# Optimization experiments

Hardware: AMD Instinct MI355X
Metric: run time of the kernel (lower is better)

The kernel has to match this reference:

```python
import jax, jax.numpy as jnp
import numpy as np

D = 128          # idim == odim
HDIM = 1024
CDIM = 128
N_ITER = HDIM // CDIM   # 8 matching-pursuit iterations
PAD = D - 1
TEMPER = 0.85
ENERGY_TH = 0.01
IGNORE_OUT = 0.0


def pad_for_shift(key):
    # key: (B,T,D) -> (B,T,S,D) windowed shift candidates, S = 2D-1
    key_pad = jnp.pad(key, ((0, 0), (0, 0), (PAD, PAD)))
    win = jnp.arange(2 * D - 1)[:, None] + jnp.arange(D)[None, :]  # (S,D)
    return key_pad[..., win]


def selector(x_aug, y):
    # cosine similarity of each shift candidate against y, argmax over shifts
    num = jnp.einsum('btsd,btd->bts', x_aug, y)
    denom = jnp.linalg.norm(x_aug, axis=-1) * jnp.linalg.norm(y, axis=-1)[..., None]
    sim = jnp.where(denom > 0, num / jnp.maximum(denom, 1e-12), 0.0)
    theta = jnp.argmax(sim, axis=-1)          # (B,T) optimal shift index
    sim_opt = jnp.max(sim, axis=-1)
    y_align = jnp.take_along_axis(x_aug, theta[..., None, None], axis=-2)[..., 0, :]
    return y_align, sim_opt, theta


def attention(x, y):
    return jax.nn.softmax(x * y / TEMPER, axis=-1)


def reverse_pad_for_shift(key, theta):
    # undo the shift selected by theta (data-dependent gather)
    key_pad = jnp.pad(key, ((0, 0), (0, 0), (PAD, PAD)))
    idx = (2 * PAD - theta)[..., None] + jnp.arange(D)  # (B,T,D)
    return jnp.take_along_axis(key_pad, idx, axis=-1)


def disentangle(x, mask_prev, W_enc, W_dec):
    # encode, pick CDIM fresh highest-energy hidden units, decode
    h = jax.nn.relu(x @ W_enc)                      # (B,T,HDIM)
    energy = jnp.mean(h * h, axis=(0, 1))           # (HDIM,)
    avail = jnp.where(mask_prev > 0, -jnp.inf, energy)
    _, idx = jax.lax.top_k(avail, CDIM)
    mask_cur = jnp.zeros((HDIM,), h.dtype).at[idx].set(1.0)
    h_sel = h * mask_cur
    out = h_sel @ W_dec
    loss_h = jnp.mean((h - h_sel) ** 2)
    return out, mask_prev + mask_cur, loss_h


def seq_energy_loss(pred, target, seq_mask, th):
    energy = jnp.mean(target * target, axis=-1)     # (B,T)
    valid = (~seq_mask) & (energy > th)[..., None]
    diff = (pred - target) ** 2 * valid
    return jnp.sum(diff) / jnp.maximum(jnp.sum(valid), 1)


def setup_inputs() -> dict:
    key = jax.random.key(0)
    k1, k2, k3, k4 = jax.random.split(key, 4)
    B, T = 8, 512
    return {
        'x': jax.random.normal(k1, (B, T, D), jnp.float32),
        'y': jax.random.normal(k2, (B, T, D), jnp.float32),
        'W_enc': jax.random.normal(k3, (D, HDIM), jnp.float32) / np.sqrt(D),
        'W_dec': jax.random.normal(k4, (HDIM, D), jnp.float32) / np.sqrt(HDIM),
    }


def reference(x, y, W_enc, W_dec):
    seq_mask = (y == IGNORE_OUT)
    y_res, x_res = y, x
    mask_prev = jnp.zeros((HDIM,), x.dtype)
    losses = []
    for _ in range(N_ITER):
        x_aug = pad_for_shift(x_res)                        # (B,T,2D-1,D)
        y_align_opt, sim_opt, theta = selector(x_aug, y_res)
        attn = attention(y_align_opt, y_res)
        y_align_opt_attn = y_align_opt * attn
        x_ele = reverse_pad_for_shift(y_align_opt_attn, theta)
        y_ele, mask_prev, loss_h = disentangle(y_align_opt_attn, mask_prev, W_enc, W_dec)
        loss_local = seq_energy_loss(y_ele, y_res, seq_mask, ENERGY_TH)
        losses.append(loss_local + loss_h)
        # .detach() in original -> stop_gradient on residuals
        y_res = jax.lax.stop_gradient(y_res - y_ele)
        x_res = jax.lax.stop_gradient(x_res - x_ele)
    return jnp.mean(jnp.stack(losses))
```

## Files before the change

kernel.cpp:

```cpp
#include <hip/hip_runtime.h>
#include <math.h>

#define DD 128
#define SS 255
#define HDIM 1024
#define CDIM 128
#define NPOS 4096
#define TEMPER 0.85f
#define ENERGY_TH 0.01f

__global__ __launch_bounds__(256) void k_init(const float* __restrict__ x, const float* __restrict__ y,
                                              float* __restrict__ xr, float* __restrict__ yr,
                                              float* __restrict__ energy, float* __restrict__ maskp,
                                              float* __restrict__ scal) {
    int gid = blockIdx.x * 256 + threadIdx.x;
    for (int i = gid; i < NPOS * DD; i += gridDim.x * 256) { xr[i] = x[i]; yr[i] = y[i]; }
    if (gid < HDIM) { energy[gid] = 0.f; maskp[gid] = 0.f; }
    if (gid < 8)    { scal[gid] = 0.f; }
}

__global__ __launch_bounds__(256) void k_align(float* __restrict__ xr_g, const float* __restrict__ yr_g,
                                               float* __restrict__ V_g) {
    __shared__ __align__(16) float xsp[4][384];
    __shared__ __align__(16) float vpad[4][384];
    __shared__ __align__(16) float ysl[4][128];
    __shared__ float Pfl[4][128];

    const int t = threadIdx.x;
    const int w = t >> 6;
    const int l = t & 63;
    const int pos = blockIdx.x * 4 + w;

    float* xs = xsp[w];
    float* vp = vpad[w];
    float* yw = ysl[w];
    float* pf = Pfl[w];

    for (int i = l; i < 127; i += 64) { xs[i] = 0.f; vp[i] = 0.f; }
    for (int i = 255 + l; i < 384; i += 64) { xs[i] = 0.f; vp[i] = 0.f; }

    const float2 x2 = *(const float2*)(xr_g + pos * DD + 2 * l);
    const float2 y2 = *(const float2*)(yr_g + pos * DD + 2 * l);
    xs[127 + 2 * l] = x2.x; xs[128 + 2 * l] = x2.y;
    yw[2 * l] = y2.x; yw[2 * l + 1] = y2.y;

    float a = x2.x * x2.x, b = x2.y * x2.y;
    float c = a + b;
    #pragma unroll
    for (int off = 1; off < 64; off <<= 1) {
        float n = __shfl_up(c, off);
        if (l >= off) c += n;
    }
    float excl = c - (a + b);
    pf[2 * l]     = excl + a;
    pf[2 * l + 1] = c;

    float yn = y2.x * y2.x + y2.y * y2.y;
    #pragma unroll
    for (int off = 32; off > 0; off >>= 1) yn += __shfl_xor(yn, off);

    __syncthreads();

    float acc0 = 0.f, acc1 = 0.f, acc2 = 0.f, acc3 = 0.f;
    const float4* xs4 = (const float4*)(xs + 4 * l);
    const float4* yw4 = (const float4*)yw;
    float4 xa = xs4[0];
    #pragma unroll 4
    for (int j = 0; j < 32; ++j) {
        float4 xb = xs4[j + 1];
        float4 yv = yw4[j];
        acc0 = fmaf(xa.x, yv.x, fmaf(xa.y, yv.y, fmaf(xa.z, yv.z, fmaf(xa.w, yv.w, acc0))));
        acc1 = fmaf(xa.y, yv.x, fmaf(xa.z, yv.y, fmaf(xa.w, yv.z, fmaf(xb.x, yv.w, acc1))));
        acc2 = fmaf(xa.z, yv.x, fmaf(xa.w, yv.y, fmaf(xb.x, yv.z, fmaf(xb.y, yv.w, acc2))));
        acc3 = fmaf(xa.w, yv.x, fmaf(xb.x, yv.y, fmaf(xb.y, yv.z, fmaf(xb.z, yv.w, acc3))));
        xa = xb;
    }

    float best = -INFINITY; int bidx = 0;
    float accs[4] = {acc0, acc1, acc2, acc3};
    #pragma unroll
    for (int k = 0; k < 4; ++k) {
        int s = 4 * l + k;
        float nrm2 = pf[s < DD ? s : DD - 1] - ((s >= DD) ? pf[s - DD] : 0.f);
        nrm2 = fmaxf(nrm2, 0.f);
        float denom = sqrtf(nrm2) * sqrtf(yn);
        float sim = (denom > 0.f) ? accs[k] / fmaxf(denom, 1e-12f) : 0.f;
        if (s == SS) sim = -INFINITY;
        if (sim > best) { best = sim; bidx = s; }
    }
    #pragma unroll
    for (int off = 32; off > 0; off >>= 1) {
        float ov = __shfl_xor(best, off);
        int   oi = __shfl_xor(bidx, off);
        if (ov > best || (ov == best && oi < bidx)) { best = ov; bidx = oi; }
    }
    const int theta = bidx;

    const int d0 = l, d1 = l + 64;
    float ya0 = xs[theta + d0], ya1 = xs[theta + d1];
    float z0 = ya0 * yw[d0] / TEMPER;
    float z1 = ya1 * yw[d1] / TEMPER;
    float zm = fmaxf(z0, z1);
    #pragma unroll
    for (int off = 32; off > 0; off >>= 1) zm = fmaxf(zm, __shfl_xor(zm, off));
    float e0 = expf(z0 - zm), e1 = expf(z1 - zm);
    float es = e0 + e1;
    #pragma unroll
    for (int off = 32; off > 0; off >>= 1) es += __shfl_xor(es, off);
    float v0 = ya0 * (e0 / es);
    float v1 = ya1 * (e1 / es);
    vp[127 + d0] = v0;
    vp[127 + d1] = v1;
    V_g[pos * DD + d0] = v0;
    V_g[pos * DD + d1] = v1;

    __syncthreads();

    float xe0 = vp[d0 + 2 * (DD - 1) - theta];
    float xe1 = vp[d1 + 2 * (DD - 1) - theta];
    xr_g[pos * DD + d0] = xs[127 + d0] - xe0;
    xr_g[pos * DD + d1] = xs[127 + d1] - xe1;
}

#define MT 64
__global__ __launch_bounds__(256) void k_energy(const float* __restrict__ V_g, const float* __restrict__ We,
                                                float* __restrict__ energy) {
    __shared__ __align__(16) float Vl[MT][DD];
    const int t  = threadIdx.x;
    const int tx = t & 63;
    const int ty = t >> 6;
    const int m0 = blockIdx.x * MT;
    const int n0 = blockIdx.y * 256;
    const int j  = n0 + tx * 4;
    const int r0 = ty * 16;

    const float4* v4 = (const float4*)(V_g + m0 * DD);
    float4* vl4 = (float4*)(&Vl[0][0]);
    #pragma unroll
    for (int i = 0; i < 8; ++i) vl4[t + 256 * i] = v4[t + 256 * i];
    __syncthreads();

    float acc[16][4];
    #pragma unroll
    for (int r = 0; r < 16; ++r)
        #pragma unroll
        for (int cc = 0; cc < 4; ++cc) acc[r][cc] = 0.f;

    for (int d0 = 0; d0 < DD; d0 += 4) {
        float wreg[4][4];
        #pragma unroll
        for (int dd = 0; dd < 4; ++dd) {
            float4 wa = *(const float4*)(We + (d0 + dd) * HDIM + j);
            wreg[dd][0] = wa.x; wreg[dd][1] = wa.y; wreg[dd][2] = wa.z; wreg[dd][3] = wa.w;
        }
        #pragma unroll
        for (int r = 0; r < 16; ++r) {
            float4 v = *(const float4*)(&Vl[r0 + r][d0]);
            float vv[4] = {v.x, v.y, v.z, v.w};
            #pragma unroll
            for (int dd = 0; dd < 4; ++dd)
                #pragma unroll
                for (int cc = 0; cc < 4; ++cc)
                    acc[r][cc] = fmaf(vv[dd], wreg[dd][cc], acc[r][cc]);
        }
    }

    __syncthreads();
    float* Ps = &Vl[0][0];
    #pragma unroll
    for (int cc = 0; cc < 4; ++cc) {
        float e = 0.f;
        #pragma unroll
        for (int r = 0; r < 16; ++r) { float h = fmaxf(acc[r][cc], 0.f); e = fmaf(h, h, e); }
        Ps[ty * 256 + tx * 4 + cc] = e;
    }
    __syncthreads();
    float esum = 0.f;
    #pragma unroll
    for (int q = 0; q < 4; ++q) esum += Ps[q * 256 + t];
    atomicAdd(&energy[n0 + t], esum);
}

__global__ __launch_bounds__(1024) void k_select(float* __restrict__ energy, float* __restrict__ maskp,
                                                 float* __restrict__ scal,
                                                 const float* __restrict__ We, const float* __restrict__ Wd,
                                                 float* __restrict__ Wes, float* __restrict__ Wds, int iter) {
    __shared__ float sv[HDIM];
    __shared__ int   si[HDIM];
    __shared__ int   mk[HDIM];
    __shared__ float red[HDIM];
    __shared__ int   sel_l[CDIM];

    const int t = threadIdx.x;
    if (t == 0) {
        if (iter > 0) scal[3] += scal[0] / fmaxf(scal[1], 1.f) + scal[2];
        scal[0] = 0.f; scal[1] = 0.f;
    }
    float e = energy[t] * (1.0f / (float)NPOS);
    sv[t] = (maskp[t] > 0.f) ? -INFINITY : e;
    si[t] = t;
    __syncthreads();

    for (int k = 2; k <= HDIM; k <<= 1) {
        for (int j = k >> 1; j > 0; j >>= 1) {
            int ixj = t ^ j;
            if (ixj > t) {
                bool up = ((t & k) == 0);
                float va = sv[t], vb = sv[ixj];
                int ia = si[t], ib = si[ixj];
                bool inorder = (va > vb) || (va == vb && ia < ib);
                if (up != inorder) { sv[t] = vb; si[t] = ib; sv[ixj] = va; si[ixj] = ia; }
            }
            __syncthreads();
        }
    }

    mk[t] = 0;
    __syncthreads();
    if (t < CDIM) { mk[si[t]] = 1; sel_l[t] = si[t]; }
    __syncthreads();
    const int mym = mk[t];

    red[t] = e;
    __syncthreads();
    for (int off = 512; off > 0; off >>= 1) { if (t < off) red[t] += red[t + off]; __syncthreads(); }
    const float sum_all = red[0];
    __syncthreads();
    red[t] = mym ? e : 0.f;
    __syncthreads();
    for (int off = 512; off > 0; off >>= 1) { if (t < off) red[t] += red[t + off]; __syncthreads(); }
    const float sum_sel = red[0];
    if (t == 0) scal[2] = (sum_all - sum_sel) / (float)HDIM;

    maskp[t] = maskp[t] + (float)mym;
    energy[t] = 0.f;
    __syncthreads();

    for (int i = t; i < DD * CDIM; i += HDIM) {
        int d = i >> 7, kk = i & 127;
        Wes[i] = We[d * HDIM + sel_l[kk]];
    }
    for (int i = t; i < CDIM * DD; i += HDIM) {
        int kk = i >> 7, d = i & 127;
        Wds[i] = Wd[sel_l[kk] * DD + d];
    }
}

#define RT 32
__global__ __launch_bounds__(256) void k_decode(const float* __restrict__ V_g, const float* __restrict__ Wes,
                                                const float* __restrict__ Wds, float* __restrict__ yr_g,
                                                const float* __restrict__ y_orig, float* __restrict__ scal) {
    __shared__ __align__(16) float Vl[RT][DD];
    __shared__ __align__(16) float Hs[RT][CDIM];
    __shared__ float ren[RT];
    __shared__ float redf[256];

    const int t = threadIdx.x;
    const int r0 = blockIdx.x * RT;

    const float4* v4 = (const float4*)(V_g + r0 * DD);
    float4* vl4 = (float4*)(&Vl[0][0]);
    #pragma unroll
    for (int i = 0; i < 4; ++i) vl4[t + 256 * i] = v4[t + 256 * i];

    {
        int r = t >> 3, lane8 = t & 7;
        float s = 0.f;
        const float* yp = yr_g + (r0 + r) * DD + lane8 * 16;
        #pragma unroll
        for (int c = 0; c < 16; ++c) { float v = yp[c]; s = fmaf(v, v, s); }
        s += __shfl_xor(s, 1); s += __shfl_xor(s, 2); s += __shfl_xor(s, 4);
        if (lane8 == 0) ren[r] = s * (1.f / (float)DD);
    }
    __syncthreads();

    const int half = t >> 7;
    const int k = t & 127;

    {
        float acc[16];
        #pragma unroll
        for (int r = 0; r < 16; ++r) acc[r] = 0.f;
        for (int d0 = 0; d0 < DD; d0 += 4) {
            float w0 = Wes[(d0 + 0) * CDIM + k];
            float w1 = Wes[(d0 + 1) * CDIM + k];
            float w2 = Wes[(d0 + 2) * CDIM + k];
            float w3 = Wes[(d0 + 3) * CDIM + k];
            #pragma unroll
            for (int r = 0; r < 16; ++r) {
                float4 v = *(const float4*)(&Vl[half * 16 + r][d0]);
                acc[r] = fmaf(v.x, w0, fmaf(v.y, w1, fmaf(v.z, w2, fmaf(v.w, w3, acc[r]))));
            }
        }
        #pragma unroll
        for (int r = 0; r < 16; ++r) Hs[half * 16 + r][k] = fmaxf(acc[r], 0.f);
    }
    __syncthreads();

    {
        float acc[16];
        #pragma unroll
        for (int r = 0; r < 16; ++r) acc[r] = 0.f;
        for (int k0 = 0; k0 < CDIM; k0 += 4) {
            float w0 = Wds[(k0 + 0) * DD + k];
            float w1 = Wds[(k0 + 1) * DD + k];
            float w2 = Wds[(k0 + 2) * DD + k];
            float w3 = Wds[(k0 + 3) * DD + k];
            #pragma unroll
            for (int r = 0; r < 16; ++r) {
                float4 h = *(const float4*)(&Hs[half * 16 + r][k0]);
                acc[r] = fmaf(h.x, w0, fmaf(h.y, w1, fmaf(h.z, w2, fmaf(h.w, w3, acc[r]))));
            }
        }
        float sd = 0.f, svld = 0.f;
        #pragma unroll
        for (int r = 0; r < 16; ++r) {
            int row = r0 + half * 16 + r;
            float tgt = yr_g[row * DD + k];
            float yo  = y_orig[row * DD + k];
            bool valid = (yo != 0.f) && (ren[half * 16 + r] > ENERGY_TH);
            float diff = acc[r] - tgt;
            if (valid) { sd = fmaf(diff, diff, sd); svld += 1.f; }
            yr_g[row * DD + k] = tgt - acc[r];
        }
        redf[t] = sd;
        __syncthreads();
        for (int off = 128; off > 0; off >>= 1) { if (t < off) redf[t] += redf[t + off]; __syncthreads(); }
        if (t == 0) atomicAdd(&scal[0], redf[0]);
        __syncthreads();
        redf[t] = svld;
        __syncthreads();
        for (int off = 128; off > 0; off >>= 1) { if (t < off) redf[t] += redf[t + off]; __syncthreads(); }
        if (t == 0) atomicAdd(&scal[1], redf[0]);
    }
}

__global__ void k_final(const float* __restrict__ scal, float* __restrict__ out) {
    float total = scal[3] + scal[0] / fmaxf(scal[1], 1.f) + scal[2];
    out[0] = total * (1.f / 8.f);
}

extern "C" void kernel_launch(void* const* d_in, const int* in_sizes, int n_in,
                              void* d_out, int out_size, void* d_ws, size_t ws_size,
                              hipStream_t stream) {
    const float* x  = (const float*)d_in[0];
    const float* y  = (const float*)d_in[1];
    const float* We = (const float*)d_in[2];
    const float* Wd = (const float*)d_in[3];

    float* ws     = (float*)d_ws;
    float* xr     = ws;
    float* yr     = ws + 524288;
    float* V      = ws + 1048576;
    float* Wes    = ws + 1572864;
    float* Wds    = ws + 1589248;
    float* energy = ws + 1605632;
    float* maskp  = ws + 1606656;
    float* scal   = ws + 1607808;
    float* out    = (float*)d_out;

    k_init<<<2048, 256, 0, stream>>>(x, y, xr, yr, energy, maskp, scal);
    for (int it = 0; it < 8; ++it) {
        k_align<<<NPOS / 4, 256, 0, stream>>>(xr, yr, V);
        k_energy<<<dim3(NPOS / MT, HDIM / 256), 256, 0, stream>>>(V, We, energy);
        k_select<<<1, 1024, 0, stream>>>(energy, maskp, scal, We, Wd, Wes, Wds, it);
        k_decode<<<NPOS / RT, 256, 0, stream>>>(V, Wes, Wds, yr, y, scal);
    }
    k_final<<<1, 1, 0, stream>>>(scal, out);
}
```

Baseline: 728.5 us.

## Fuse all matching-pursuit iterations into one cooperative persistent kernel

Replaces the per-iteration launches of align, energy, select and decode with a single cooperative kernel of 256 blocks that uses grid.sync between phases. Each block owns 16 rows, so V stays in shared memory instead of round-tripping through global memory. Top-k is done in parallel by rank counting across blocks, and energy, mask and loss buffers are double-buffered by iteration parity. This removes around 33 kernel launches and the single-block select bottleneck. In exchange it adds grid-wide barriers and gives the energy GEMM only 256 blocks, each with large per-thread register accumulators. A fallback path keeps the old multi-kernel sequence if the cooperative launch fails.

Result: slower. 1.141 ms (+56.6%).

```diff
diff --git a/kernel.cpp b/kernel.cpp
--- a/kernel.cpp
+++ b/kernel.cpp
@@ -1,5 +1,8 @@
 #include <hip/hip_runtime.h>
+#include <hip/hip_cooperative_groups.h>
 #include <math.h>
+
+namespace cg = cooperative_groups;
 
 #define DD 128
 #define SS 255
@@ -8,6 +11,312 @@
 #define NPOS 4096
 #define TEMPER 0.85f
 #define ENERGY_TH 0.01f
+#define NBLK 256
+#define RPB 16
+
+__global__ __launch_bounds__(256)
+void k_mega(const float* __restrict__ x, const float* __restrict__ y,
+            const float* __restrict__ We, const float* __restrict__ Wd,
+            float* __restrict__ xr, float* __restrict__ yr,
+            float* __restrict__ Wes, float* __restrict__ Wds,
+            float* __restrict__ energy,
+            float* __restrict__ maskp,
+            float* __restrict__ scal,
+            unsigned int* __restrict__ selcnt,
+            float* __restrict__ out)
+{
+    cg::grid_group grid = cg::this_grid();
+    const int b = blockIdx.x;
+    const int t = threadIdx.x;
+    const int w = t >> 6, l = t & 63;
+
+    __shared__ __align__(16) float Vl[RPB][DD];
+    __shared__ __align__(16) float xsp[4][384];
+    __shared__ __align__(16) float vpad[4][384];
+    __shared__ __align__(16) float ysl[4][128];
+    __shared__ float Pfl[4][128];
+    __shared__ __align__(16) float Hs[RPB][CDIM];
+    __shared__ float ren[RPB];
+    __shared__ float redl[8];
+    __shared__ float avL[HDIM];
+    __shared__ unsigned int rkL[4];
+    __shared__ int selSlot[4];
+    __shared__ int selFlag[4];
+
+    {
+        const int r0 = b * RPB;
+        const float4* xs4g = (const float4*)(x + (size_t)r0 * DD);
+        const float4* ys4g = (const float4*)(y + (size_t)r0 * DD);
+        float4* xr4 = (float4*)(xr + (size_t)r0 * DD);
+        float4* yr4 = (float4*)(yr + (size_t)r0 * DD);
+        xr4[t] = xs4g[t]; xr4[t + 256] = xs4g[t + 256];
+        yr4[t] = ys4g[t]; yr4[t + 256] = ys4g[t + 256];
+        if (t < 4) {
+            energy[0 * HDIM + 4 * b + t] = 0.f;
+            energy[1 * HDIM + 4 * b + t] = 0.f;
+            maskp[1 * HDIM + 4 * b + t] = 0.f;
+        }
+        if (b == 0) {
+            if (t < 8) scal[t] = 0.f;
+            if (t < 2) selcnt[t] = 0u;
+        }
+    }
+    grid.sync();
+
+    for (int it = 0; it < 8; ++it) {
+        const int p = it & 1, pp = p ^ 1;
+
+        float* xs = xsp[w]; float* vp = vpad[w]; float* yw = ysl[w]; float* pf = Pfl[w];
+        for (int i = l; i < 127; i += 64)        { xs[i] = 0.f; vp[i] = 0.f; }
+        for (int i = 255 + l; i < 384; i += 64)  { xs[i] = 0.f; vp[i] = 0.f; }
+
+        for (int pq = 0; pq < 4; ++pq) {
+            const int r = 4 * w + pq;
+            const int pos = b * RPB + r;
+            const float2 x2 = *(const float2*)(xr + (size_t)pos * DD + 2 * l);
+            const float2 y2 = *(const float2*)(yr + (size_t)pos * DD + 2 * l);
+            xs[127 + 2 * l] = x2.x; xs[128 + 2 * l] = x2.y;
+            yw[2 * l] = y2.x; yw[2 * l + 1] = y2.y;
+
+            float a = x2.x * x2.x, bb = x2.y * x2.y;
+            float c = a + bb;
+            #pragma unroll
+            for (int off = 1; off < 64; off <<= 1) {
+                float n = __shfl_up(c, off);
+                if (l >= off) c += n;
+            }
+            float excl = c - (a + bb);
+            pf[2 * l] = excl + a;
+            pf[2 * l + 1] = c;
+            float ynv = y2.x * y2.x + y2.y * y2.y;
+            #pragma unroll
+            for (int off = 32; off > 0; off >>= 1) ynv += __shfl_xor(ynv, off);
+            __syncthreads();
+
+            float acc0 = 0.f, acc1 = 0.f, acc2 = 0.f, acc3 = 0.f;
+            const float4* xs4 = (const float4*)(xs + 4 * l);
+            const float4* yw4 = (const float4*)yw;
+            float4 xa = xs4[0];
+            #pragma unroll 4
+            for (int j = 0; j < 32; ++j) {
+                float4 xb = xs4[j + 1];
+                float4 yv = yw4[j];
+                acc0 = fmaf(xa.x, yv.x, fmaf(xa.y, yv.y, fmaf(xa.z, yv.z, fmaf(xa.w, yv.w, acc0))));
+                acc1 = fmaf(xa.y, yv.x, fmaf(xa.z, yv.y, fmaf(xa.w, yv.z, fmaf(xb.x, yv.w, acc1))));
+                acc2 = fmaf(xa.z, yv.x, fmaf(xa.w, yv.y, fmaf(xb.x, yv.z, fmaf(xb.y, yv.w, acc2))));
+                acc3 = fmaf(xa.w, yv.x, fmaf(xb.x, yv.y, fmaf(xb.y, yv.z, fmaf(xb.z, yv.w, acc3))));
+                xa = xb;
+            }
+            float best = -INFINITY; int bidx = 0;
+            float accs[4] = {acc0, acc1, acc2, acc3};
+            #pragma unroll
+            for (int q = 0; q < 4; ++q) {
+                int s = 4 * l + q;
+                float nrm2 = pf[s < DD ? s : DD - 1] - ((s >= DD) ? pf[s - DD] : 0.f);
+                nrm2 = fmaxf(nrm2, 0.f);
+                float denom = sqrtf(nrm2) * sqrtf(ynv);
+                float sim = (denom > 0.f) ? accs[q] / fmaxf(denom, 1e-12f) : 0.f;
+                if (s == SS) sim = -INFINITY;
+                if (sim > best) { best = sim; bidx = s; }
+            }
+            #pragma unroll
+            for (int off = 32; off > 0; off >>= 1) {
+                float ov = __shfl_xor(best, off);
+                int   oi = __shfl_xor(bidx, off);
+                if (ov > best || (ov == best && oi < bidx)) { best = ov; bidx = oi; }
+            }
+            const int theta = bidx;
+
+            float ya0 = xs[theta + l], ya1 = xs[theta + l + 64];
+            float z0 = ya0 * yw[l] / TEMPER;
+            float z1 = ya1 * yw[l + 64] / TEMPER;
+            float zm = fmaxf(z0, z1);
+            #pragma unroll
+            for (int off = 32; off > 0; off >>= 1) zm = fmaxf(zm, __shfl_xor(zm, off));
+            float e0 = expf(z0 - zm), e1 = expf(z1 - zm);
+            float es = e0 + e1;
+            #pragma unroll
+            for (int off = 32; off > 0; off >>= 1) es += __shfl_xor(es, off);
+            float v0 = ya0 * (e0 / es);
+            float v1 = ya1 * (e1 / es);
+            vp[127 + l] = v0; vp[127 + l + 64] = v1;
+            Vl[r][l] = v0;    Vl[r][l + 64] = v1;
+            __syncthreads();
+
+            float xe0 = vp[l + 2 * (DD - 1) - theta];
+            float xe1 = vp[l + 64 + 2 * (DD - 1) - theta];
+            xr[(size_t)pos * DD + l]      = xs[127 + l] - xe0;
+            xr[(size_t)pos * DD + l + 64] = xs[127 + l + 64] - xe1;
+        }
+        __syncthreads();
+
+        {
+            float acc[RPB][4];
+            #pragma unroll
+            for (int r = 0; r < RPB; ++r)
+                #pragma unroll
+                for (int cc = 0; cc < 4; ++cc) acc[r][cc] = 0.f;
+
+            for (int d0 = 0; d0 < DD; d0 += 4) {
+                float4 wr[4];
+                #pragma unroll
+                for (int dd = 0; dd < 4; ++dd)
+                    wr[dd] = *(const float4*)(We + (size_t)(d0 + dd) * HDIM + 4 * t);
+                #pragma unroll
+                for (int r = 0; r < RPB; ++r) {
+                    float4 v = *(const float4*)(&Vl[r][d0]);
+                    const float vv[4] = {v.x, v.y, v.z, v.w};
+                    #pragma unroll
+                    for (int dd = 0; dd < 4; ++dd) {
+                        const float* wp = (const float*)&wr[dd];
+                        #pragma unroll
+                        for (int cc = 0; cc < 4; ++cc)
+                            acc[r][cc] = fmaf(vv[dd], wp[cc], acc[r][cc]);
+                    }
+                }
+            }
+            #pragma unroll
+            for (int cc = 0; cc < 4; ++cc) {
+                float e = 0.f;
+                #pragma unroll
+                for (int r = 0; r < RPB; ++r) { float h = fmaxf(acc[r][cc], 0.f); e = fmaf(h, h, e); }
+                atomicAdd(&energy[p * HDIM + 4 * t + cc], e);
+            }
+        }
+        grid.sync();
+
+        {
+            for (int i = t; i < HDIM; i += 256) {
+                float e = energy[p * HDIM + i];
+                float m = maskp[pp * HDIM + i];
+                avL[i] = (m > 0.f) ? -INFINITY : e;
+            }
+            if (t < 4) rkL[t] = 0u;
+            __syncthreads();
+
+            const int i0 = 4 * b;
+            unsigned int cnt[4] = {0u, 0u, 0u, 0u};
+            const float av0 = avL[i0], av1 = avL[i0 + 1], av2 = avL[i0 + 2], av3 = avL[i0 + 3];
+            #pragma unroll
+            for (int jj = 0; jj < 4; ++jj) {
+                int j = t + 256 * jj;
+                float aj = avL[j];
+                cnt[0] += (aj > av0) || (aj == av0 && j < i0);
+                cnt[1] += (aj > av1) || (aj == av1 && j < i0 + 1);
+                cnt[2] += (aj > av2) || (aj == av2 && j < i0 + 2);
+                cnt[3] += (aj > av3) || (aj == av3 && j < i0 + 3);
+            }
+            #pragma unroll
+            for (int q = 0; q < 4; ++q) if (cnt[q]) atomicAdd(&rkL[q], cnt[q]);
+            __syncthreads();
+
+            if (t < 4) {
+                const int i = i0 + t;
+                const bool masked = (avL[i] == -INFINITY);
+                const bool sel = (rkL[t] < 128u) && !masked;
+                maskp[p * HDIM + i] = (masked || sel) ? 1.f : 0.f;
+                energy[pp * HDIM + i] = 0.f;
+                int slot = -1;
+                if (sel) slot = (int)atomicAdd(&selcnt[p], 1u);
+                selFlag[t] = sel ? 1 : 0;
+                selSlot[t] = slot;
+                if (!sel) atomicAdd(&scal[4 + p], energy[p * HDIM + i]);
+            }
+            if (b == 0 && t == 0) {
+                scal[6] += scal[0 + pp] / fmaxf(scal[2 + pp], 1.f)
+                         + scal[4 + pp] * (1.f / (4096.f * 1024.f));
+                scal[0 + pp] = 0.f; scal[2 + pp] = 0.f; scal[4 + pp] = 0.f;
+                selcnt[pp] = 0u;
+            }
+            __syncthreads();
+
+            #pragma unroll
+            for (int q = 0; q < 4; ++q) {
+                if (selFlag[q]) {
+                    const int i = i0 + q, slot = selSlot[q];
+                    if (t < 128) Wes[(size_t)t * CDIM + slot] = We[(size_t)t * HDIM + i];
+                    else { int d = t - 128; Wds[(size_t)slot * DD + d] = Wd[(size_t)i * DD + d]; }
+                }
+            }
+        }
+        grid.sync();
+
+        {
+            const int r0g = b * RPB;
+            {
+                int r = t >> 4, ln = t & 15;
+                float s = 0.f;
+                const float* yp = yr + (size_t)(r0g + r) * DD + ln * 8;
+                #pragma unroll
+                for (int cci = 0; cci < 8; ++cci) { float v = yp[cci]; s = fmaf(v, v, s); }
+                s += __shfl_xor(s, 1); s += __shfl_xor(s, 2);
+                s += __shfl_xor(s, 4); s += __shfl_xor(s, 8);
+                if (ln == 0) ren[r] = s * (1.f / (float)DD);
+            }
+            const int k = t & 127, rg = t >> 7;
+
+            float acc1[8];
+            #pragma unroll
+            for (int r = 0; r < 8; ++r) acc1[r] = 0.f;
+            for (int d0 = 0; d0 < DD; d0 += 4) {
+                float w0 = Wes[(size_t)(d0 + 0) * CDIM + k];
+                float w1 = Wes[(size_t)(d0 + 1) * CDIM + k];
+                float w2 = Wes[(size_t)(d0 + 2) * CDIM + k];
+                float w3 = Wes[(size_t)(d0 + 3) * CDIM + k];
+                #pragma unroll
+                for (int r = 0; r < 8; ++r) {
+                    float4 v = *(const float4*)(&Vl[rg * 8 + r][d0]);
+                    acc1[r] = fmaf(v.x, w0, fmaf(v.y, w1, fmaf(v.z, w2, fmaf(v.w, w3, acc1[r]))));
+                }
+            }
+            #pragma unroll
+            for (int r = 0; r < 8; ++r) Hs[rg * 8 + r][k] = fmaxf(acc1[r], 0.f);
+            __syncthreads();
+
+            float acc2[8];
+            #pragma unroll
+            for (int r = 0; r < 8; ++r) acc2[r] = 0.f;
+            for (int k0 = 0; k0 < CDIM; k0 += 4) {
+                float w0 = Wds[(size_t)(k0 + 0) * DD + k];
+                float w1 = Wds[(size_t)(k0 + 1) * DD + k];
+                float w2 = Wds[(size_t)(k0 + 2) * DD + k];
+                float w3 = Wds[(size_t)(k0 + 3) * DD + k];
+                #pragma unroll
+                for (int r = 0; r < 8; ++r) {
+                    float4 h = *(const float4*)(&Hs[rg * 8 + r][k0]);
+                    acc2[r] = fmaf(h.x, w0, fmaf(h.y, w1, fmaf(h.z, w2, fmaf(h.w, w3, acc2[r]))));
+                }
+            }
+            float sd = 0.f, sv = 0.f;
+            #pragma unroll
+            for (int r = 0; r < 8; ++r) {
+                const int row = r0g + rg * 8 + r;
+                float tgt = yr[(size_t)row * DD + k];
+                float yo  = y [(size_t)row * DD + k];
+                bool valid = (yo != 0.f) && (ren[rg * 8 + r] > ENERGY_TH);
+                float diff = acc2[r] - tgt;
+                if (valid) { sd = fmaf(diff, diff, sd); sv += 1.f; }
+                yr[(size_t)row * DD + k] = tgt - acc2[r];
+            }
+            #pragma unroll
+            for (int off = 32; off > 0; off >>= 1) { sd += __shfl_xor(sd, off); sv += __shfl_xor(sv, off); }
+            if (l == 0) { redl[w] = sd; redl[4 + w] = sv; }
+            __syncthreads();
+            if (t == 0) {
+                atomicAdd(&scal[0 + p], redl[0] + redl[1] + redl[2] + redl[3]);
+                atomicAdd(&scal[2 + p], redl[4] + redl[5] + redl[6] + redl[7]);
+            }
+            __threadfence_block();
+            __syncthreads();
+        }
+    }
+    grid.sync();
+    if (b == 0 && t == 0) {
+        float total = scal[6] + scal[1] / fmaxf(scal[3], 1.f)
+                    + scal[5] * (1.f / (4096.f * 1024.f));
+        out[0] = total * 0.125f;
+    }
+}
 
 __global__ __launch_bounds__(256) void k_init(const float* __restrict__ x, const float* __restrict__ y,
                                               float* __restrict__ xr, float* __restrict__ yr,
@@ -27,14 +336,10 @@
     __shared__ float Pfl[4][128];
 
     const int t = threadIdx.x;
-    const int w = t >> 6;
-    const int l = t & 63;
+    const int w = t >> 6, l = t & 63;
     const int pos = blockIdx.x * 4 + w;
 
-    float* xs = xsp[w];
-    float* vp = vpad[w];
-    float* yw = ysl[w];
-    float* pf = Pfl[w];
+    float* xs = xsp[w]; float* vp = vpad[w]; float* yw = ysl[w]; float* pf = Pfl[w];
 
     for (int i = l; i < 127; i += 64) { xs[i] = 0.f; vp[i] = 0.f; }
     for (int i = 255 + l; i < 384; i += 64) { xs[i] = 0.f; vp[i] = 0.f; }
@@ -52,13 +357,12 @@
         if (l >= off) c += n;
     }
     float excl = c - (a + b);
-    pf[2 * l]     = excl + a;
+    pf[2 * l] = excl + a;
     pf[2 * l + 1] = c;
 
     float yn = y2.x * y2.x + y2.y * y2.y;
     #pragma unroll
     for (int off = 32; off > 0; off >>= 1) yn += __shfl_xor(yn, off);
-
     __syncthreads();
 
     float acc0 = 0.f, acc1 = 0.f, acc2 = 0.f, acc3 = 0.f;
@@ -79,12 +383,12 @@
     float best = -INFINITY; int bidx = 0;
     float accs[4] = {acc0, acc1, acc2, acc3};
     #pragma unroll
-    for (int k = 0; k < 4; ++k) {
-        int s = 4 * l + k;
+    for (int q = 0; q < 4; ++q) {
+        int s = 4 * l + q;
         float nrm2 = pf[s < DD ? s : DD - 1] - ((s >= DD) ? pf[s - DD] : 0.f);
         nrm2 = fmaxf(nrm2, 0.f);
         float denom = sqrtf(nrm2) * sqrtf(yn);
-        float sim = (denom > 0.f) ? accs[k] / fmaxf(denom, 1e-12f) : 0.f;
+        float sim = (denom > 0.f) ? accs[q] / fmaxf(denom, 1e-12f) : 0.f;
         if (s == SS) sim = -INFINITY;
         if (sim > best) { best = sim; bidx = s; }
     }
@@ -109,11 +413,8 @@
     for (int off = 32; off > 0; off >>= 1) es += __shfl_xor(es, off);
     float v0 = ya0 * (e0 / es);
     float v1 = ya1 * (e1 / es);
-    vp[127 + d0] = v0;
-    vp[127 + d1] = v1;
-    V_g[pos * DD + d0] = v0;
-    V_g[pos * DD + d1] = v1;
-
+    vp[127 + d0] = v0; vp[127 + d1] = v1;
+    V_g[pos * DD + d0] = v0; V_g[pos * DD + d1] = v1;
     __syncthreads();
 
     float xe0 = vp[d0 + 2 * (DD - 1) - theta];
@@ -122,14 +423,14 @@
     xr_g[pos * DD + d1] = xs[127 + d1] - xe1;
 }
 
-#define MT 64
+#define FMT 64
 __global__ __launch_bounds__(256) void k_energy(const float* __restrict__ V_g, const float* __restrict__ We,
                                                 float* __restrict__ energy) {
-    __shared__ __align__(16) float Vl[MT][DD];
+    __shared__ __align__(16) float Vl[FMT][DD];
     const int t  = threadIdx.x;
     const int tx = t & 63;
     const int ty = t >> 6;
-    const int m0 = blockIdx.x * MT;
+    const int m0 = blockIdx.x * FMT;
     const int n0 = blockIdx.y * 256;
     const int j  = n0 + tx * 4;
     const int r0 = ty * 16;
@@ -351,20 +652,35 @@
     float* ws     = (float*)d_ws;
     float* xr     = ws;
     float* yr     = ws + 524288;
-    float* V      = ws + 1048576;
-    float* Wes    = ws + 1572864;
-    float* Wds    = ws + 1589248;
-    float* energy = ws + 1605632;
-    float* maskp  = ws + 1606656;
-    float* scal   = ws + 1607808;
+    float* Wes    = ws + 1048576;
+    float* Wds    = ws + 1064960;
+    float* energy = ws + 1081344;
+    float* maskp  = ws + 1083392;
+    float* scal   = ws + 1085440;
+    unsigned int* selcnt = (unsigned int*)(ws + 1085448);
+    float* V       = ws + 1081344;
+    float* fenergy = ws + 1605632;
+    float* fmaskp  = ws + 1606656;
+    float* fscal   = ws + 1607680;
     float* out    = (float*)d_out;
 
-    k_init<<<2048, 256, 0, stream>>>(x, y, xr, yr, energy, maskp, scal);
-    for (int it = 0; it < 8; ++it) {
-        k_align<<<NPOS / 4, 256, 0, stream>>>(xr, yr, V);
-        k_energy<<<dim3(NPOS / MT, HDIM / 256), 256, 0, stream>>>(V, We, energy);
-        k_select<<<1, 1024, 0, stream>>>(energy, maskp, scal, We, Wd, Wes, Wds, it);
-        k_decode<<<NPOS / RT, 256, 0, stream>>>(V, Wes, Wds, yr, y, scal);
-    }
-    k_final<<<1, 1, 0, stream>>>(scal, out);
-}
+    void* args[] = {
+        (void*)&x, (void*)&y, (void*)&We, (void*)&Wd,
+        (void*)&xr, (void*)&yr, (void*)&Wes, (void*)&Wds,
+        (void*)&energy, (void*)&maskp, (void*)&scal, (void*)&selcnt,
+        (void*)&out
+    };
+    hipError_t err = hipLaunchCooperativeKernel((const void*)k_mega, dim3(NBLK),
+                                                dim3(256), args, 0u, stream);
+    if (err != hipSuccess) {
+        (void)hipGetLastError();
+        k_init<<<2048, 256, 0, stream>>>(x, y, xr, yr, fenergy, fmaskp, fscal);
+        for (int it = 0; it < 8; ++it) {
+            k_align<<<NPOS / 4, 256, 0, stream>>>(xr, yr, V);
+            k_energy<<<dim3(NPOS / FMT, HDIM / 256), 256, 0, stream>>>(V, We, fenergy);
+            k_select<<<1, 1024, 0, stream>>>(fenergy, fmaskp, fscal, We, Wd, Wes, Wds, it);
+            k_decode<<<NPOS / RT, 256, 0, stream>>>(V, Wes, Wds, yr, y, fscal);
+        }
+        k_final<<<1, 1, 0, stream>>>(fscal, out);
+    }
+}
```

## Fuse top-k selection into energy kernel and next alignment into decode

Applied to the files above, without the earlier changes.

The selection step now runs inside the energy GEMM kernel, in whichever block finishes last, found through an atomic counter. This removes the separate single-block select launch. The decode kernel is templated so it also runs the next iteration's shift alignment on rows it just produced, reading the updated residual from shared memory. The initial copy of x and y into the workspace is dropped, because the first alignment reads the inputs directly. The cost is fewer rows per decode block, alignment running serially across 4 positions per wave, and a 256-thread bitonic sort in the last block.

New measurement: 919.2 us. 26.2% more time.

```diff
diff --git a/kernel.cpp b/kernel.cpp
--- a/kernel.cpp
+++ b/kernel.cpp
@@ -8,39 +8,33 @@
 #define NPOS 4096
 #define TEMPER 0.85f
 #define ENERGY_TH 0.01f
-
-__global__ __launch_bounds__(256) void k_init(const float* __restrict__ x, const float* __restrict__ y,
-                                              float* __restrict__ xr, float* __restrict__ yr,
-                                              float* __restrict__ energy, float* __restrict__ maskp,
-                                              float* __restrict__ scal) {
-    int gid = blockIdx.x * 256 + threadIdx.x;
-    for (int i = gid; i < NPOS * DD; i += gridDim.x * 256) { xr[i] = x[i]; yr[i] = y[i]; }
-    if (gid < HDIM) { energy[gid] = 0.f; maskp[gid] = 0.f; }
-    if (gid < 8)    { scal[gid] = 0.f; }
-}
-
-__global__ __launch_bounds__(256) void k_align(float* __restrict__ xr_g, const float* __restrict__ yr_g,
-                                               float* __restrict__ V_g) {
+#define FMT 64
+
+__global__ __launch_bounds__(1024) void k_init0(float* __restrict__ energy, float* __restrict__ maskp,
+                                                float* __restrict__ scal, unsigned int* __restrict__ counter) {
+    const int t = threadIdx.x;
+    energy[t] = 0.f; maskp[t] = 0.f;
+    if (t < 8) { scal[t] = 0.f; counter[t] = 0u; }
+}
+
+__global__ __launch_bounds__(256) void k_align0(const float* __restrict__ x_in, const float* __restrict__ y_in,
+                                                float* __restrict__ xr_g, float* __restrict__ V_g) {
     __shared__ __align__(16) float xsp[4][384];
     __shared__ __align__(16) float vpad[4][384];
     __shared__ __align__(16) float ysl[4][128];
     __shared__ float Pfl[4][128];
 
     const int t = threadIdx.x;
-    const int w = t >> 6;
-    const int l = t & 63;
+    const int w = t >> 6, l = t & 63;
     const int pos = blockIdx.x * 4 + w;
 
-    float* xs = xsp[w];
-    float* vp = vpad[w];
-    float* yw = ysl[w];
-    float* pf = Pfl[w];
+    float* xs = xsp[w]; float* vp = vpad[w]; float* yw = ysl[w]; float* pf = Pfl[w];
 
     for (int i = l; i < 127; i += 64) { xs[i] = 0.f; vp[i] = 0.f; }
     for (int i = 255 + l; i < 384; i += 64) { xs[i] = 0.f; vp[i] = 0.f; }
 
-    const float2 x2 = *(const float2*)(xr_g + pos * DD + 2 * l);
-    const float2 y2 = *(const float2*)(yr_g + pos * DD + 2 * l);
+    const float2 x2 = *(const float2*)(x_in + (size_t)pos * DD + 2 * l);
+    const float2 y2 = *(const float2*)(y_in + (size_t)pos * DD + 2 * l);
     xs[127 + 2 * l] = x2.x; xs[128 + 2 * l] = x2.y;
     yw[2 * l] = y2.x; yw[2 * l + 1] = y2.y;
 
@@ -52,13 +46,12 @@
         if (l >= off) c += n;
     }
     float excl = c - (a + b);
-    pf[2 * l]     = excl + a;
+    pf[2 * l] = excl + a;
     pf[2 * l + 1] = c;
 
     float yn = y2.x * y2.x + y2.y * y2.y;
     #pragma unroll
     for (int off = 32; off > 0; off >>= 1) yn += __shfl_xor(yn, off);
-
     __syncthreads();
 
     float acc0 = 0.f, acc1 = 0.f, acc2 = 0.f, acc3 = 0.f;
@@ -79,12 +72,12 @@
     float best = -INFINITY; int bidx = 0;
     float accs[4] = {acc0, acc1, acc2, acc3};
     #pragma unroll
-    for (int k = 0; k < 4; ++k) {
-        int s = 4 * l + k;
+    for (int q = 0; q < 4; ++q) {
+        int s = 4 * l + q;
         float nrm2 = pf[s < DD ? s : DD - 1] - ((s >= DD) ? pf[s - DD] : 0.f);
         nrm2 = fmaxf(nrm2, 0.f);
         float denom = sqrtf(nrm2) * sqrtf(yn);
-        float sim = (denom > 0.f) ? accs[k] / fmaxf(denom, 1e-12f) : 0.f;
+        float sim = (denom > 0.f) ? accs[q] / fmaxf(denom, 1e-12f) : 0.f;
         if (s == SS) sim = -INFINITY;
         if (sim > best) { best = sim; bidx = s; }
     }
@@ -109,32 +102,32 @@
     for (int off = 32; off > 0; off >>= 1) es += __shfl_xor(es, off);
     float v0 = ya0 * (e0 / es);
     float v1 = ya1 * (e1 / es);
-    vp[127 + d0] = v0;
-    vp[127 + d1] = v1;
-    V_g[pos * DD + d0] = v0;
-    V_g[pos * DD + d1] = v1;
-
+    vp[127 + d0] = v0; vp[127 + d1] = v1;
+    V_g[(size_t)pos * DD + d0] = v0; V_g[(size_t)pos * DD + d1] = v1;
     __syncthreads();
 
     float xe0 = vp[d0 + 2 * (DD - 1) - theta];
     float xe1 = vp[d1 + 2 * (DD - 1) - theta];
-    xr_g[pos * DD + d0] = xs[127 + d0] - xe0;
-    xr_g[pos * DD + d1] = xs[127 + d1] - xe1;
-}
-
-#define MT 64
-__global__ __launch_bounds__(256) void k_energy(const float* __restrict__ V_g, const float* __restrict__ We,
-                                                float* __restrict__ energy) {
-    __shared__ __align__(16) float Vl[MT][DD];
+    xr_g[(size_t)pos * DD + d0] = xs[127 + d0] - xe0;
+    xr_g[(size_t)pos * DD + d1] = xs[127 + d1] - xe1;
+}
+
+__global__ __launch_bounds__(256) void k_es(const float* __restrict__ V_g, const float* __restrict__ We,
+                                            const float* __restrict__ Wd,
+                                            float* __restrict__ energy, float* __restrict__ maskp,
+                                            float* __restrict__ scal,
+                                            float* __restrict__ Wes, float* __restrict__ Wds,
+                                            unsigned int* __restrict__ counter, int iter) {
+    __shared__ __align__(16) float Vl[FMT][DD];
     const int t  = threadIdx.x;
     const int tx = t & 63;
     const int ty = t >> 6;
-    const int m0 = blockIdx.x * MT;
+    const int m0 = blockIdx.x * FMT;
     const int n0 = blockIdx.y * 256;
     const int j  = n0 + tx * 4;
     const int r0 = ty * 16;
 
-    const float4* v4 = (const float4*)(V_g + m0 * DD);
+    const float4* v4 = (const float4*)(V_g + (size_t)m0 * DD);
     float4* vl4 = (float4*)(&Vl[0][0]);
     #pragma unroll
     for (int i = 0; i < 8; ++i) vl4[t + 256 * i] = v4[t + 256 * i];
@@ -150,7 +143,7 @@
         float wreg[4][4];
         #pragma unroll
         for (int dd = 0; dd < 4; ++dd) {
-            float4 wa = *(const float4*)(We + (d0 + dd) * HDIM + j);
+            float4 wa = *(const float4*)(We + (size_t)(d0 + dd) * HDIM + j);
             wreg[dd][0] = wa.x; wreg[dd][1] = wa.y; wreg[dd][2] = wa.z; wreg[dd][3] = wa.w;
         }
         #pragma unroll
@@ -179,98 +172,116 @@
     #pragma unroll
     for (int q = 0; q < 4; ++q) esum += Ps[q * 256 + t];
     atomicAdd(&energy[n0 + t], esum);
-}
-
-__global__ __launch_bounds__(1024) void k_select(float* __restrict__ energy, float* __restrict__ maskp,
-                                                 float* __restrict__ scal,
-                                                 const float* __restrict__ We, const float* __restrict__ Wd,
-                                                 float* __restrict__ Wes, float* __restrict__ Wds, int iter) {
-    __shared__ float sv[HDIM];
-    __shared__ int   si[HDIM];
-    __shared__ int   mk[HDIM];
-    __shared__ float red[HDIM];
-    __shared__ int   sel_l[CDIM];
-
-    const int t = threadIdx.x;
+
+    __threadfence();
+    __shared__ unsigned int lastFlag;
+    if (t == 0) {
+        unsigned int prev = atomicAdd(counter, 1u);
+        lastFlag = (prev == 64u * 4u - 1u) ? 1u : 0u;
+    }
+    __syncthreads();
+    if (!lastFlag) return;
+
+    float* sv = &Vl[0][0];
+    int*   si = (int*)&Vl[8][0];
+    float* ev = &Vl[16][0];
+    float* red = &Vl[24][0];
+    __shared__ int sel_l[CDIM];
+
     if (t == 0) {
         if (iter > 0) scal[3] += scal[0] / fmaxf(scal[1], 1.f) + scal[2];
         scal[0] = 0.f; scal[1] = 0.f;
     }
-    float e = energy[t] * (1.0f / (float)NPOS);
-    sv[t] = (maskp[t] > 0.f) ? -INFINITY : e;
-    si[t] = t;
+    #pragma unroll
+    for (int q = 0; q < 4; ++q) {
+        int i = t + 256 * q;
+        float e = atomicAdd(&energy[i], 0.f) * (1.0f / (float)NPOS);
+        ev[i] = e;
+        sv[i] = (maskp[i] > 0.f) ? -INFINITY : e;
+        si[i] = i;
+    }
     __syncthreads();
 
     for (int k = 2; k <= HDIM; k <<= 1) {
-        for (int j = k >> 1; j > 0; j >>= 1) {
-            int ixj = t ^ j;
-            if (ixj > t) {
-                bool up = ((t & k) == 0);
-                float va = sv[t], vb = sv[ixj];
-                int ia = si[t], ib = si[ixj];
-                bool inorder = (va > vb) || (va == vb && ia < ib);
-                if (up != inorder) { sv[t] = vb; si[t] = ib; sv[ixj] = va; si[ixj] = ia; }
+        for (int jj = k >> 1; jj > 0; jj >>= 1) {
+            #pragma unroll
+            for (int q = 0; q < 4; ++q) {
+                int e = t + 256 * q;
+                int ixj = e ^ jj;
+                if (ixj > e) {
+                    bool up = ((e & k) == 0);
+                    float va = sv[e], vb = sv[ixj];
+                    int ia = si[e], ib = si[ixj];
+                    bool inorder = (va > vb) || (va == vb && ia < ib);
+                    if (up != inorder) { sv[e] = vb; si[e] = ib; sv[ixj] = va; si[ixj] = ia; }
+                }
             }
             __syncthreads();
         }
     }
 
-    mk[t] = 0;
-    __syncthreads();
-    if (t < CDIM) { mk[si[t]] = 1; sel_l[t] = si[t]; }
-    __syncthreads();
-    const int mym = mk[t];
-
-    red[t] = e;
-    __syncthreads();
-    for (int off = 512; off > 0; off >>= 1) { if (t < off) red[t] += red[t + off]; __syncthreads(); }
+    if (t < CDIM) {
+        int s = si[t];
+        sel_l[t] = s;
+        maskp[s] = maskp[s] + 1.f;
+    }
+    #pragma unroll
+    for (int q = 0; q < 4; ++q) energy[t + 256 * q] = 0.f;
+
+    float pa = 0.f;
+    #pragma unroll
+    for (int q = 0; q < 4; ++q) pa += ev[t + 256 * q];
+    red[t] = pa;
+    __syncthreads();
+    for (int off = 128; off > 0; off >>= 1) { if (t < off) red[t] += red[t + off]; __syncthreads(); }
     const float sum_all = red[0];
     __syncthreads();
-    red[t] = mym ? e : 0.f;
-    __syncthreads();
-    for (int off = 512; off > 0; off >>= 1) { if (t < off) red[t] += red[t + off]; __syncthreads(); }
-    const float sum_sel = red[0];
-    if (t == 0) scal[2] = (sum_all - sum_sel) / (float)HDIM;
-
-    maskp[t] = maskp[t] + (float)mym;
-    energy[t] = 0.f;
-    __syncthreads();
-
-    for (int i = t; i < DD * CDIM; i += HDIM) {
+    red[t] = (t < CDIM) ? ev[sel_l[t]] : 0.f;
+    __syncthreads();
+    for (int off = 128; off > 0; off >>= 1) { if (t < off) red[t] += red[t + off]; __syncthreads(); }
+    if (t == 0) scal[2] = (sum_all - red[0]) / (float)HDIM;
+    __syncthreads();
+
+    for (int i = t; i < DD * CDIM; i += 256) {
         int d = i >> 7, kk = i & 127;
-        Wes[i] = We[d * HDIM + sel_l[kk]];
-    }
-    for (int i = t; i < CDIM * DD; i += HDIM) {
+        Wes[i] = We[(size_t)d * HDIM + sel_l[kk]];
+    }
+    for (int i = t; i < CDIM * DD; i += 256) {
         int kk = i >> 7, d = i & 127;
-        Wds[i] = Wd[sel_l[kk] * DD + d];
-    }
-}
-
-#define RT 32
-__global__ __launch_bounds__(256) void k_decode(const float* __restrict__ V_g, const float* __restrict__ Wes,
-                                                const float* __restrict__ Wds, float* __restrict__ yr_g,
-                                                const float* __restrict__ y_orig, float* __restrict__ scal) {
-    __shared__ __align__(16) float Vl[RT][DD];
-    __shared__ __align__(16) float Hs[RT][CDIM];
-    __shared__ float ren[RT];
+        Wds[i] = Wd[(size_t)sel_l[kk] * DD + d];
+    }
+}
+
+template<int FIRST, int DO_ALIGN>
+__global__ __launch_bounds__(256) void k_da(const float* __restrict__ V_g, const float* __restrict__ Wes,
+                                            const float* __restrict__ Wds, float* __restrict__ yr_g,
+                                            const float* __restrict__ y_orig, float* __restrict__ scal,
+                                            float* __restrict__ xr_g, float* __restrict__ V_out) {
+    __shared__ __align__(16) float Vl[16][DD];
+    __shared__ __align__(16) float Hs[16][CDIM];
+    __shared__ __align__(16) float yblk[16][DD];
+    __shared__ float ren[16];
     __shared__ float redf[256];
-
-    const int t = threadIdx.x;
-    const int r0 = blockIdx.x * RT;
-
-    const float4* v4 = (const float4*)(V_g + r0 * DD);
+    __shared__ __align__(16) float xsp[4][384];
+    __shared__ __align__(16) float vpad[4][384];
+    __shared__ float Pfl[4][128];
+
+    const int t = threadIdx.x, w = t >> 6, l = t & 63;
+    const int r0 = blockIdx.x * 16;
+    const float* ycur = FIRST ? y_orig : yr_g;
+
+    const float4* v4 = (const float4*)(V_g + (size_t)r0 * DD);
     float4* vl4 = (float4*)(&Vl[0][0]);
-    #pragma unroll
-    for (int i = 0; i < 4; ++i) vl4[t + 256 * i] = v4[t + 256 * i];
+    vl4[t] = v4[t]; vl4[t + 256] = v4[t + 256];
 
     {
-        int r = t >> 3, lane8 = t & 7;
+        int r = t >> 4, ln = t & 15;
         float s = 0.f;
-        const float* yp = yr_g + (r0 + r) * DD + lane8 * 16;
-        #pragma unroll
-        for (int c = 0; c < 16; ++c) { float v = yp[c]; s = fmaf(v, v, s); }
-        s += __shfl_xor(s, 1); s += __shfl_xor(s, 2); s += __shfl_xor(s, 4);
-        if (lane8 == 0) ren[r] = s * (1.f / (float)DD);
+        const float* yp = ycur + (size_t)(r0 + r) * DD + ln * 8;
+        #pragma unroll
+        for (int c = 0; c < 8; ++c) { float v = yp[c]; s = fmaf(v, v, s); }
+        s += __shfl_xor(s, 1); s += __shfl_xor(s, 2); s += __shfl_xor(s, 4); s += __shfl_xor(s, 8);
+        if (ln == 0) ren[r] = s * (1.f / (float)DD);
     }
     __syncthreads();
 
@@ -278,60 +289,150 @@
     const int k = t & 127;
 
     {
-        float acc[16];
-        #pragma unroll
-        for (int r = 0; r < 16; ++r) acc[r] = 0.f;
+        float acc[8];
+        #pragma unroll
+        for (int r = 0; r < 8; ++r) acc[r] = 0.f;
         for (int d0 = 0; d0 < DD; d0 += 4) {
-            float w0 = Wes[(d0 + 0) * CDIM + k];
-            float w1 = Wes[(d0 + 1) * CDIM + k];
-            float w2 = Wes[(d0 + 2) * CDIM + k];
-            float w3 = Wes[(d0 + 3) * CDIM + k];
-            #pragma unroll
-            for (int r = 0; r < 16; ++r) {
-                float4 v = *(const float4*)(&Vl[half * 16 + r][d0]);
+            float w0 = Wes[(size_t)(d0 + 0) * CDIM + k];
+            float w1 = Wes[(size_t)(d0 + 1) * CDIM + k];
+            float w2 = Wes[(size_t)(d0 + 2) * CDIM + k];
+            float w3 = Wes[(size_t)(d0 + 3) * CDIM + k];
+            #pragma unroll
+            for (int r = 0; r < 8; ++r) {
+                float4 v = *(const float4*)(&Vl[half * 8 + r][d0]);
                 acc[r] = fmaf(v.x, w0, fmaf(v.y, w1, fmaf(v.z, w2, fmaf(v.w, w3, acc[r]))));
             }
         }
         #pragma unroll
-        for (int r = 0; r < 16; ++r) Hs[half * 16 + r][k] = fmaxf(acc[r], 0.f);
+        for (int r = 0; r < 8; ++r) Hs[half * 8 + r][k] = fmaxf(acc[r], 0.f);
     }
     __syncthreads();
 
     {
-        float acc[16];
-        #pragma unroll
-        for (int r = 0; r < 16; ++r) acc[r] = 0.f;
+        float acc[8];
+        #pragma unroll
+        for (int r = 0; r < 8; ++r) acc[r] = 0.f;
         for (int k0 = 0; k0 < CDIM; k0 += 4) {
-            float w0 = Wds[(k0 + 0) * DD + k];
-            float w1 = Wds[(k0 + 1) * DD + k];
-            float w2 = Wds[(k0 + 2) * DD + k];
-            float w3 = Wds[(k0 + 3) * DD + k];
-            #pragma unroll
-            for (int r = 0; r < 16; ++r) {
-                float4 h = *(const float4*)(&Hs[half * 16 + r][k0]);
+            float w0 = Wds[(size_t)(k0 + 0) * DD + k];
+            float w1 = Wds[(size_t)(k0 + 1) * DD + k];
+            float w2 = Wds[(size_t)(k0 + 2) * DD + k];
+            float w3 = Wds[(size_t)(k0 + 3) * DD + k];
+            #pragma unroll
+            for (int r = 0; r < 8; ++r) {
+                float4 h = *(const float4*)(&Hs[half * 8 + r][k0]);
                 acc[r] = fmaf(h.x, w0, fmaf(h.y, w1, fmaf(h.z, w2, fmaf(h.w, w3, acc[r]))));
             }
         }
-        float sd = 0.f, svld = 0.f;
-        #pragma unroll
-        for (int r = 0; r < 16; ++r) {
-            int row = r0 + half * 16 + r;
-            float tgt = yr_g[row * DD + k];
-            float yo  = y_orig[row * DD + k];
-            bool valid = (yo != 0.f) && (ren[half * 16 + r] > ENERGY_TH);
+        float sd = 0.f, sv = 0.f;
+        #pragma unroll
+        for (int r = 0; r < 8; ++r) {
+            const int row = r0 + half * 8 + r;
+            float tgt = ycur[(size_t)row * DD + k];
+            float yo  = y_orig[(size_t)row * DD + k];
+            bool valid = (yo != 0.f) && (ren[half * 8 + r] > ENERGY_TH);
             float diff = acc[r] - tgt;
-            if (valid) { sd = fmaf(diff, diff, sd); svld += 1.f; }
-            yr_g[row * DD + k] = tgt - acc[r];
+            if (valid) { sd = fmaf(diff, diff, sd); sv += 1.f; }
+            float ny = tgt - acc[r];
+            yr_g[(size_t)row * DD + k] = ny;
+            yblk[half * 8 + r][k] = ny;
         }
         redf[t] = sd;
         __syncthreads();
         for (int off = 128; off > 0; off >>= 1) { if (t < off) redf[t] += redf[t + off]; __syncthreads(); }
         if (t == 0) atomicAdd(&scal[0], redf[0]);
         __syncthreads();
-        redf[t] = svld;
+        redf[t] = sv;
         __syncthreads();
         for (int off = 128; off > 0; off >>= 1) { if (t < off) redf[t] += redf[t + off]; __syncthreads(); }
         if (t == 0) atomicAdd(&scal[1], redf[0]);
+        __syncthreads();
+    }
+
+    if (DO_ALIGN) {
+        float* xs = xsp[w]; float* vp = vpad[w]; float* pf = Pfl[w];
+        for (int i = l; i < 127; i += 64) { xs[i] = 0.f; vp[i] = 0.f; }
+        for (int i = 255 + l; i < 384; i += 64) { xs[i] = 0.f; vp[i] = 0.f; }
+
+        for (int pq = 0; pq < 4; ++pq) {
+            const int r = 4 * w + pq;
+            const int pos = r0 + r;
+            const float* yw = yblk[r];
+            const float2 x2 = *(const float2*)(xr_g + (size_t)pos * DD + 2 * l);
+            xs[127 + 2 * l] = x2.x; xs[128 + 2 * l] = x2.y;
+            const float y0v = yw[2 * l], y1v = yw[2 * l + 1];
+
+            float a = x2.x * x2.x, bb = x2.y * x2.y;
+            float c = a + bb;
+            #pragma unroll
+            for (int off = 1; off < 64; off <<= 1) {
+                float n = __shfl_up(c, off);
+                if (l >= off) c += n;
+            }
+            float excl = c - (a + bb);
+            pf[2 * l] = excl + a;
+            pf[2 * l + 1] = c;
+            float ynv = y0v * y0v + y1v * y1v;
+            #pragma unroll
+            for (int off = 32; off > 0; off >>= 1) ynv += __shfl_xor(ynv, off);
+            __syncthreads();
+
+            float acc0 = 0.f, acc1 = 0.f, acc2 = 0.f, acc3 = 0.f;
+            const float4* xs4 = (const float4*)(xs + 4 * l);
+            const float4* yw4 = (const float4*)yw;
+            float4 xa = xs4[0];
+            #pragma unroll 4
+            for (int jj = 0; jj < 32; ++jj) {
+                float4 xb = xs4[jj + 1];
+                float4 yv = yw4[jj];
+                acc0 = fmaf(xa.x, yv.x, fmaf(xa.y, yv.y, fmaf(xa.z, yv.z, fmaf(xa.w, yv.w, acc0))));
+                acc1 = fmaf(xa.y, yv.x, fmaf(xa.z, yv.y, fmaf(xa.w, yv.z, fmaf(xb.x, yv.w, acc1))));
+                acc2 = fmaf(xa.z, yv.x, fmaf(xa.w, yv.y, fmaf(xb.x, yv.z, fmaf(xb.y, yv.w, acc2))));
+                acc3 = fmaf(xa.w, yv.x, fmaf(xb.x, yv.y, fmaf(xb.y, yv.z, fmaf(xb.z, yv.w, acc3))));
+                xa = xb;
+            }
+            float best = -INFINITY; int bidx = 0;
+            float accs[4] = {acc0, acc1, acc2, acc3};
+            #pragma unroll
+            for (int q = 0; q < 4; ++q) {
+                int s = 4 * l + q;
+                float nrm2 = pf[s < DD ? s : DD - 1] - ((s >= DD) ? pf[s - DD] : 0.f);
+                nrm2 = fmaxf(nrm2, 0.f);
+                float denom = sqrtf(nrm2) * sqrtf(ynv);
+                float sim = (denom > 0.f) ? accs[q] / fmaxf(denom, 1e-12f) : 0.f;
+                if (s == SS) sim = -INFINITY;
+                if (sim > best) { best = sim; bidx = s; }
+            }
+            #pragma unroll
+            for (int off = 32; off > 0; off >>= 1) {
+                float ov = __shfl_xor(best, off);
+                int   oi = __shfl_xor(bidx, off);
+                if (ov > best || (ov == best && oi < bidx)) { best = ov; bidx = oi; }
+            }
+            const int theta = bidx;
+
+            float ya0 = xs[theta + l], ya1 = xs[theta + l + 64];
+            float z0 = ya0 * yw[l] / TEMPER;
+            float z1 = ya1 * yw[l + 64] / TEMPER;
+            float zm = fmaxf(z0, z1);
+            #pragma unroll
+            for (int off = 32; off > 0; off >>= 1) zm = fmaxf(zm, __shfl_xor(zm, off));
+            float e0 = expf(z0 - zm), e1 = expf(z1 - zm);
+            float es = e0 + e1;
+            #pragma unroll
+            for (int off = 32; off > 0; off >>= 1) es += __shfl_xor(es, off);
+            float v0 = ya0 * (e0 / es);
+            float v1 = ya1 * (e1 / es);
+            vp[127 + l] = v0; vp[127 + l + 64] = v1;
+            V_out[(size_t)pos * DD + l] = v0;
+            V_out[(size_t)pos * DD + l + 64] = v1;
+            __syncthreads();
+
+            float xe0 = vp[l + 2 * (DD - 1) - theta];
+            float xe1 = vp[l + 64 + 2 * (DD - 1) - theta];
+            xr_g[(size_t)pos * DD + l]      = xs[127 + l] - xe0;
+            xr_g[(size_t)pos * DD + l + 64] = xs[127 + l + 64] - xe1;
+            __syncthreads();
+        }
     }
 }
 
@@ -356,15 +457,18 @@
     float* Wds    = ws + 1589248;
     float* energy = ws + 1605632;
     float* maskp  = ws + 1606656;
-    float* scal   = ws + 1607808;
+    float* scal   = ws + 1607680;
+    unsigned int* counter = (unsigned int*)(ws + 1607688);
     float* out    = (float*)d_out;
 
-    k_init<<<2048, 256, 0, stream>>>(x, y, xr, yr, energy, maskp, scal);
+    k_init0<<<1, 1024, 0, stream>>>(energy, maskp, scal, counter);
+    k_align0<<<NPOS / 4, 256, 0, stream>>>(x, y, xr, V);
     for (int it = 0; it < 8; ++it) {
-        k_align<<<NPOS / 4, 256, 0, stream>>>(xr, yr, V);
-        k_energy<<<dim3(NPOS / MT, HDIM / 256), 256, 0, stream>>>(V, We, energy);
-        k_select<<<1, 1024, 0, stream>>>(energy, maskp, scal, We, Wd, Wes, Wds, it);
-        k_decode<<<NPOS / RT, 256, 0, stream>>>(V, Wes, Wds, yr, y, scal);
+        k_es<<<dim3(NPOS / FMT, HDIM / 256), 256, 0, stream>>>(V, We, Wd, energy, maskp,
+                                                               scal, Wes, Wds, counter + it, it);
+        if (it == 0)      k_da<1, 1><<<NPOS / 16, 256, 0, stream>>>(V, Wes, Wds, yr, y, scal, xr, V);
+        else if (it < 7)  k_da<0, 1><<<NPOS / 16, 256, 0, stream>>>(V, Wes, Wds, yr, y, scal, xr, V);
+        else              k_da<0, 0><<<NPOS / 16, 256, 0, stream>>>(V, Wes, Wds, yr, y, scal, xr, V);
     }
     k_final<<<1, 1, 0, stream>>>(scal, out);
 }
```
